# Performance work log

Measured on AMD Instinct MI355X. Metric: run time of the kernel, lower is better.

Reference implementation:

```python
import jax, jax.numpy as jnp
import numpy as np

N, E, B, EP = 100000, 1600000, 512, 200000
NIN, NEMB, HID, NL = 64, 64, 72, 3
EPS = 1e-5


def setup_inputs() -> dict:
    key = jax.random.key(0)
    ks = jax.random.split(key, 20)
    inp = {
        'x': jax.random.normal(ks[0], (N, NIN), jnp.float32),
        'emb': jax.random.normal(ks[1], (N, NEMB), jnp.float32),
        'assign': jax.random.uniform(ks[2], (N, B), jnp.float32),
        'edge_index': jax.random.randint(ks[3], (2, E), 0, N, jnp.int64),
        'pedge_index': jax.random.randint(ks[4], (2, EP), 0, B, jnp.int64),
        # params (xavier-ish scale)
        'node_w': jax.random.normal(ks[5], (NIN, HID), jnp.float32) / np.sqrt(NIN),
        'node_b': jnp.zeros((HID,), jnp.float32),
        'emb_w': jax.random.normal(ks[6], (NEMB, HID), jnp.float32) / np.sqrt(NEMB),
        'emb_b': jnp.zeros((HID,), jnp.float32),
        'conv_winit': jax.random.normal(ks[7], (NL, HID, HID), jnp.float32) / np.sqrt(HID),
        'conv_wroot': jax.random.normal(ks[8], (NL, HID, HID), jnp.float32) / np.sqrt(HID),
        'conv_bias': jnp.zeros((NL, HID), jnp.float32),
        'bn_gamma': jnp.ones((NL, HID), jnp.float32),
        'bn_beta': jnp.zeros((NL, HID), jnp.float32),
        'mlp_w1': jax.random.normal(ks[9], (12 * HID, HID), jnp.float32) / np.sqrt(12 * HID),
        'mlp_b1': jnp.zeros((HID,), jnp.float32),
        'mlp_w2': jax.random.normal(ks[10], (HID, 1), jnp.float32) / np.sqrt(HID),
        'mlp_b2': jnp.zeros((1,), jnp.float32),
    }
    return inp


def _forward(x, emb, assign, node_w, node_b, emb_w, emb_b, conv_winit,
             conv_wroot, conv_bias, bn_gamma, bn_beta, mlp_w1, mlp_b1,
             mlp_w2, mlp_b2, edge_index, pedge_index):
    n = x.shape[0]
    nb = assign.shape[1]
    row, col = edge_index[0], edge_index[1]
    # gcn_norm without self-loops (ARMAConv): D^{-1/2} A D^{-1/2}
    deg = jax.ops.segment_sum(jnp.ones((row.shape[0],), x.dtype), col, num_segments=n)
    dis = jnp.where(deg > 0, jax.lax.rsqrt(jnp.maximum(deg, 1.0)) * jnp.where(deg > 0, 1.0, 0.0), 0.0)
    dis = jnp.where(deg > 0, deg ** -0.5, 0.0)
    norm = dis[row] * dis[col]

    h = jax.nn.relu(x @ node_w + node_b)  # [N, HID]
    for l in range(NL):
        # ARMAConv K=1, T=1: relu(A_hat (h Wi) + h Wr + b)
        m = norm[:, None] * (h @ conv_winit[l])[row]        # [E, HID]
        agg = jax.ops.segment_sum(m, col, num_segments=n)   # [N, HID]
        h = jax.nn.relu(agg + h @ conv_wroot[l] + conv_bias[l])
        # F.relu applied again in forward (idempotent), then BatchNorm (training stats)
        mu = h.mean(0)
        var = ((h - mu) ** 2).mean(0)
        h = (h - mu) * jax.lax.rsqrt(var + EPS) * bn_gamma[l] + bn_beta[l]

    e = jax.nn.relu(emb @ emb_w + emb_b)
    z = jnp.concatenate([h, e], axis=-1)  # [N, 2*HID]

    batch = jnp.argmax(assign, axis=-1)
    cnt = jax.ops.segment_sum(jnp.ones((n,), z.dtype), batch, num_segments=nb)
    p1 = jax.ops.segment_sum(z, batch, num_segments=nb)
    p2 = jax.ops.segment_max(z, batch, num_segments=nb)
    p3 = p1 / jnp.maximum(cnt, 1.0)[:, None]
    xp = jnp.concatenate([p1, p2, p3], axis=-1)  # [B, 6*HID]

    pair = jnp.concatenate([xp[pedge_index[0]], xp[pedge_index[1]]], axis=1)  # [EP, 12*HID]
    out = jnp.tanh(pair @ mlp_w1 + mlp_b1) @ mlp_w2 + mlp_b2
    return out


def reference(x, emb, assign, edge_index, pedge_index, node_w, node_b, emb_w,
              emb_b, conv_winit, conv_wroot, conv_bias, bn_gamma, bn_beta,
              mlp_w1, mlp_b1, mlp_w2, mlp_b2):
    return _forward(x, emb, assign, node_w, node_b, emb_w, emb_b, conv_winit,
                    conv_wroot, conv_bias, bn_gamma, bn_beta, mlp_w1, mlp_b1,
                    mlp_w2, mlp_b2, edge_index, pedge_index)
```

## Files before the change

kernel.cpp:

```cpp
#include <hip/hip_runtime.h>
#include <hip/hip_bf16.h>

#define HID 72
#define EPSV 1e-5f
#define CAP 64

__device__ __forceinline__ float tanh_fast(float x) {
    float cx = fminf(fmaxf(x, -15.f), 15.f);
    float e = __expf(2.f * cx);
    return __fdividef(e - 1.f, e + 1.f);
}
__device__ __forceinline__ void fma4(float4& a, float w, const float4 v) {
    a.x += w * v.x; a.y += w * v.y; a.z += w * v.z; a.w += w * v.w;
}

__global__ void k_init(int* deg, float* stats, int* bcnt, int N, int statlen, int B) {
    int i = blockIdx.x * blockDim.x + threadIdx.x;
    if (i < N) deg[i] = 0;
    if (i < statlen) stats[i] = 0.f;
    if (i < B) bcnt[i] = 0;
}

__global__ __launch_bounds__(256) void k_fillcap(const int* __restrict__ row, const int* __restrict__ col,
                                                 int* __restrict__ deg, int* __restrict__ csr_r, int E) {
    int e = blockIdx.x * blockDim.x + threadIdx.x;
    if (e < E) {
        int c = col[e];
        int pos = atomicAdd(&deg[c], 1);
        if (pos < CAP) csr_r[(size_t)c * CAP + pos] = row[e];
    }
}

__global__ void k_dis(const int* __restrict__ deg, float* __restrict__ dis, int N) {
    int i = blockIdx.x * blockDim.x + threadIdx.x;
    if (i < N) {
        int d = deg[i];
        dis[i] = (d > 0) ? rsqrtf((float)d) : 0.f;
    }
}

#define DP 76
template <int K>
__global__ __launch_bounds__(256) void k_dense_t(const float* __restrict__ xin, const float* __restrict__ W,
                                                 const float* __restrict__ bias, float* __restrict__ out, int N) {
    __shared__ float hs[128][DP];
    __shared__ float ws[HID][DP];
    int tid = threadIdx.x;
    int n0 = blockIdx.x * 128;
    for (int i = tid; i < K * HID; i += 256) {
        int k = i / HID, f = i % HID;
        ws[f][k] = W[i];
    }
    for (int i = tid; i < 128 * K; i += 256) {
        int n = i / K, f = i % K;
        int gn = n0 + n;
        hs[n][f] = (gn < N) ? xin[(size_t)gn * K + f] : 0.f;
    }
    __syncthreads();
    int tn = tid & 31;
    int tf = (tid >> 5) * 9;
    float acc[4][9];
    #pragma unroll
    for (int j = 0; j < 9; j++) {
        float b = bias[tf + j];
        acc[0][j] = b; acc[1][j] = b; acc[2][j] = b; acc[3][j] = b;
    }
    #pragma unroll 2
    for (int k4 = 0; k4 < K / 4; k4++) {
        int k = k4 * 4;
        float4 h0 = *(const float4*)&hs[tn][k];
        float4 h1 = *(const float4*)&hs[tn + 32][k];
        float4 h2 = *(const float4*)&hs[tn + 64][k];
        float4 h3 = *(const float4*)&hs[tn + 96][k];
        #pragma unroll
        for (int j = 0; j < 9; j++) {
            float4 w = *(const float4*)&ws[tf + j][k];
            acc[0][j] += h0.x * w.x + h0.y * w.y + h0.z * w.z + h0.w * w.w;
            acc[1][j] += h1.x * w.x + h1.y * w.y + h1.z * w.z + h1.w * w.w;
            acc[2][j] += h2.x * w.x + h2.y * w.y + h2.z * w.z + h2.w * w.w;
            acc[3][j] += h3.x * w.x + h3.y * w.y + h3.z * w.z + h3.w * w.w;
        }
    }
    #pragma unroll
    for (int i = 0; i < 4; i++) {
        int gn = n0 + tn + 32 * i;
        if (gn >= N) continue;
        float* dst = out + (size_t)gn * HID + tf;
        #pragma unroll
        for (int j = 0; j < 9; j++) dst[j] = fmaxf(acc[i][j], 0.f);
    }
}

#define CP 76
template <bool BN>
__global__ __launch_bounds__(256) void k_conv_t(const float* t, const float* __restrict__ stats,
                                                const float* __restrict__ gamma, const float* __restrict__ beta,
                                                const float* __restrict__ wi, const float* __restrict__ wr,
                                                const float* __restrict__ cb, float* __restrict__ hw,
                                                float* agg, int N, float invN) {
    __shared__ float hs[64][CP];
    __shared__ float ws[2 * HID][CP];
    int tid = threadIdx.x;
    int n0 = blockIdx.x * 64;
    for (int i = tid; i < HID * 2 * HID; i += 256) {
        int k = i / (2 * HID), f = i % (2 * HID);
        ws[f][k] = (f < HID) ? wi[k * HID + f] : wr[k * HID + (f - HID)];
    }
    for (int i = tid; i < 64 * HID; i += 256) {
        int n = i / HID, f = i % HID;
        int gn = n0 + n;
        float v = (gn < N) ? t[(size_t)gn * HID + f] : 0.f;
        if constexpr (BN) {
            float mu = stats[f] * invN;
            float var = stats[HID + f] * invN - mu * mu;
            v = (v - mu) * rsqrtf(var + EPSV) * gamma[f] + beta[f];
        }
        hs[n][f] = v;
    }
    __syncthreads();
    int tn = tid & 15;
    int tf = (tid >> 4) * 9;
    float acc[4][9];
    #pragma unroll
    for (int j = 0; j < 9; j++) {
        float b = (tf >= HID) ? cb[tf - HID + j] : 0.f;
        acc[0][j] = b; acc[1][j] = b; acc[2][j] = b; acc[3][j] = b;
    }
    #pragma unroll 2
    for (int k4 = 0; k4 < HID / 4; k4++) {
        int k = k4 * 4;
        float4 h0 = *(const float4*)&hs[tn][k];
        float4 h1 = *(const float4*)&hs[tn + 16][k];
        float4 h2 = *(const float4*)&hs[tn + 32][k];
        float4 h3 = *(const float4*)&hs[tn + 48][k];
        #pragma unroll
        for (int j = 0; j < 9; j++) {
            float4 w = *(const float4*)&ws[tf + j][k];
            acc[0][j] += h0.x * w.x + h0.y * w.y + h0.z * w.z + h0.w * w.w;
            acc[1][j] += h1.x * w.x + h1.y * w.y + h1.z * w.z + h1.w * w.w;
            acc[2][j] += h2.x * w.x + h2.y * w.y + h2.z * w.z + h2.w * w.w;
            acc[3][j] += h3.x * w.x + h3.y * w.y + h3.z * w.z + h3.w * w.w;
        }
    }
    #pragma unroll
    for (int i = 0; i < 4; i++) {
        int gn = n0 + tn + 16 * i;
        if (gn >= N) continue;
        float* dst = (tf < HID) ? (hw + (size_t)gn * HID + tf) : (agg + (size_t)gn * HID + (tf - HID));
        #pragma unroll
        for (int j = 0; j < 9; j++) dst[j] = acc[i][j];
    }
}

__global__ __launch_bounds__(256) void k_gather9(const float* __restrict__ hw, const int* __restrict__ deg,
                                                 const int* __restrict__ csr_r, const float* __restrict__ dis,
                                                 float* t, int N) {
    int tid = blockIdx.x * blockDim.x + threadIdx.x;
    int n = tid / 9;
    int s = tid - n * 9;
    if (n >= N) return;
    float4* trow = (float4*)(t + (size_t)n * HID) + s * 2;
    float4 a0 = trow[0], a1 = trow[1];
    int d = deg[n];
    d = (d > CAP) ? CAP : d;
    float disc = dis[n];
    const int* crow = csr_r + (size_t)n * CAP;
    const float4* hb = (const float4*)hw + s * 2;
    for (int j0 = 0; j0 < d; j0 += 4) {
        int4 rr = *(const int4*)(crow + j0);
        int rem = d - j0;
        {
            float w = disc * dis[rr.x];
            const float4* hp = hb + (size_t)rr.x * 18;
            fma4(a0, w, hp[0]); fma4(a1, w, hp[1]);
        }
        if (rem > 1) {
            float w = disc * dis[rr.y];
            const float4* hp = hb + (size_t)rr.y * 18;
            fma4(a0, w, hp[0]); fma4(a1, w, hp[1]);
        }
        if (rem > 2) {
            float w = disc * dis[rr.z];
            const float4* hp = hb + (size_t)rr.z * 18;
            fma4(a0, w, hp[0]); fma4(a1, w, hp[1]);
        }
        if (rem > 3) {
            float w = disc * dis[rr.w];
            const float4* hp = hb + (size_t)rr.w * 18;
            fma4(a0, w, hp[0]); fma4(a1, w, hp[1]);
        }
    }
    trow[0] = make_float4(fmaxf(a0.x, 0.f), fmaxf(a0.y, 0.f), fmaxf(a0.z, 0.f), fmaxf(a0.w, 0.f));
    trow[1] = make_float4(fmaxf(a1.x, 0.f), fmaxf(a1.y, 0.f), fmaxf(a1.z, 0.f), fmaxf(a1.w, 0.f));
}

__global__ __launch_bounds__(256) void k_stats(const float* __restrict__ t, float* __restrict__ st, int total4) {
    __shared__ float s1[HID], s2[HID];
    int tx = threadIdx.x;
    if (tx < HID) s1[tx] = 0.f;
    else if (tx < 2 * HID) s2[tx - HID] = 0.f;
    __syncthreads();
    int stride = gridDim.x * blockDim.x;
    int i0 = blockIdx.x * blockDim.x + tx;
    int f0 = (i0 * 4) % HID;
    float a0 = 0, a1 = 0, a2 = 0, a3 = 0, q0 = 0, q1 = 0, q2 = 0, q3 = 0;
    const float4* tp = (const float4*)t;
    for (int i = i0; i < total4; i += stride) {
        float4 v = tp[i];
        a0 += v.x; q0 += v.x * v.x;
        a1 += v.y; q1 += v.y * v.y;
        a2 += v.z; q2 += v.z * v.z;
        a3 += v.w; q3 += v.w * v.w;
    }
    atomicAdd(&s1[f0 + 0], a0); atomicAdd(&s2[f0 + 0], q0);
    atomicAdd(&s1[f0 + 1], a1); atomicAdd(&s2[f0 + 1], q1);
    atomicAdd(&s1[f0 + 2], a2); atomicAdd(&s2[f0 + 2], q2);
    atomicAdd(&s1[f0 + 3], a3); atomicAdd(&s2[f0 + 3], q3);
    __syncthreads();
    if (tx < HID) {
        atomicAdd(&st[tx], s1[tx]);
        atomicAdd(&st[HID + tx], s2[tx]);
    }
}

__global__ __launch_bounds__(256) void k_argmax(const float* __restrict__ assign, int* __restrict__ batchv,
                                                int* __restrict__ bcnt, int N, int B) {
    int wib = threadIdx.x >> 6;
    int lane = threadIdx.x & 63;
    int n = blockIdx.x * (blockDim.x >> 6) + wib;
    if (n >= N) return;
    const float4* rp4 = (const float4*)(assign + (size_t)n * B);
    float best = -INFINITY;
    int bidx = 0x7fffffff;
    int nq = B / 4;
    for (int q = lane; q < nq; q += 64) {
        float4 v = rp4[q];
        int j = q * 4;
        if (v.x > best) { best = v.x; bidx = j; }
        if (v.y > best) { best = v.y; bidx = j + 1; }
        if (v.z > best) { best = v.z; bidx = j + 2; }
        if (v.w > best) { best = v.w; bidx = j + 3; }
    }
    #pragma unroll
    for (int off = 32; off > 0; off >>= 1) {
        float ov = __shfl_down(best, off);
        int oi = __shfl_down(bidx, off);
        if (ov > best || (ov == best && oi < bidx)) { best = ov; bidx = oi; }
    }
    if (lane == 0) {
        batchv[n] = bidx;
        atomicAdd(&bcnt[bidx], 1);
    }
}

__global__ __launch_bounds__(1024) void k_bscan(const int* __restrict__ bcnt, int* __restrict__ boffs,
                                                int* __restrict__ bcur, int B) {
    __shared__ int lds[1024];
    int t = threadIdx.x;
    int v = (t < B) ? bcnt[t] : 0;
    lds[t] = v;
    __syncthreads();
    for (int off = 1; off < 1024; off <<= 1) {
        int x = (t >= off) ? lds[t - off] : 0;
        __syncthreads();
        lds[t] += x;
        __syncthreads();
    }
    if (t < B) {
        int excl = lds[t] - v;
        boffs[t] = excl;
        bcur[t] = excl;
    }
}

__global__ void k_bfill(const int* __restrict__ batchv, int* __restrict__ bcur, int* __restrict__ nlist, int N) {
    int n = blockIdx.x * blockDim.x + threadIdx.x;
    if (n < N) {
        int b = batchv[n];
        int pos = atomicAdd(&bcur[b], 1);
        nlist[pos] = n;
    }
}

__global__ __launch_bounds__(576) void k_poolB(const float* __restrict__ t2, const float* __restrict__ ebuf,
                                               const float* __restrict__ stats2, const float* __restrict__ g2,
                                               const float* __restrict__ bt2, const int* __restrict__ boffs,
                                               const int* __restrict__ bcnt, const int* __restrict__ nlist,
                                               float* __restrict__ xp, float invN) {
    __shared__ float ls[4][2 * HID], lm[4][2 * HID];
    int b = blockIdx.x;
    int tid = threadIdx.x;
    int f = tid % (2 * HID);
    int ch = tid / (2 * HID);
    bool isH = f < HID;
    float a = 1.f, sh = 0.f;
    const float* src;
    if (isH) {
        float s1v = stats2[f], s2v = stats2[HID + f];
        float mu = s1v * invN;
        float var = s2v * invN - mu * mu;
        float inv = rsqrtf(var + EPSV);
        a = inv * g2[f];
        sh = bt2[f] - mu * a;
        src = t2 + f;
    } else {
        src = ebuf + (f - HID);
    }
    int s = boffs[b];
    int c = bcnt[b];
    int e = s + c;
    float sum = 0.f, mx = -INFINITY;
    for (int i = s + ch; i < e; i += 4) {
        float v = src[(size_t)nlist[i] * HID] * a + sh;
        sum += v;
        mx = fmaxf(mx, v);
    }
    ls[ch][f] = sum;
    lm[ch][f] = mx;
    __syncthreads();
    if (ch == 0) {
        float stot = ls[0][f] + ls[1][f] + ls[2][f] + ls[3][f];
        float mtot = fmaxf(fmaxf(lm[0][f], lm[1][f]), fmaxf(lm[2][f], lm[3][f]));
        float* xr = xp + (size_t)b * (6 * HID);
        xr[f] = stot;
        xr[2 * HID + f] = mtot;
        xr[4 * HID + f] = stot / fmaxf((float)c, 1.f);
    }
}

__global__ __launch_bounds__(192) void k_uv(const float* __restrict__ xp, const float* __restrict__ w1,
                                            const float* __restrict__ b1, float* __restrict__ U,
                                            float* __restrict__ V) {
    int b = blockIdx.x;
    int t = threadIdx.x;
    if (t >= 2 * HID) return;
    int half = t / HID;
    int f = t % HID;
    const float* xr = xp + (size_t)b * (6 * HID);
    const float* wb = w1 + (size_t)half * (6 * HID) * HID + f;
    float acc = (half == 0) ? b1[f] : 0.f;
    #pragma unroll 4
    for (int k = 0; k < 6 * HID; k++) acc += xr[k] * wb[(size_t)k * HID];
    if (half == 0) U[(size_t)b * HID + f] = acc;
    else           V[(size_t)b * HID + f] = acc;
}

__global__ __launch_bounds__(256) void k_edge(const int* __restrict__ pe, const float* __restrict__ U,
                                              const float* __restrict__ V, const float* __restrict__ w2,
                                              const float* __restrict__ b2, float* __restrict__ out, int EP) {
    int ep = blockIdx.x * blockDim.x + threadIdx.x;
    if (ep >= EP) return;
    int a = pe[ep];
    int b = pe[EP + ep];
    const float4* up = (const float4*)(U + (size_t)a * HID);
    const float4* vp = (const float4*)(V + (size_t)b * HID);
    float s = 0.f;
    #pragma unroll
    for (int q = 0; q < HID / 4; q++) {
        float4 u = up[q];
        float4 v = vp[q];
        s += tanh_fast(u.x + v.x) * w2[q * 4 + 0];
        s += tanh_fast(u.y + v.y) * w2[q * 4 + 1];
        s += tanh_fast(u.z + v.z) * w2[q * 4 + 2];
        s += tanh_fast(u.w + v.w) * w2[q * 4 + 3];
    }
    out[ep] = s + b2[0];
}

extern "C" void kernel_launch(void* const* d_in, const int* in_sizes, int n_in,
                              void* d_out, int out_size, void* d_ws, size_t ws_size,
                              hipStream_t stream) {
    const float* x       = (const float*)d_in[0];
    const float* emb     = (const float*)d_in[1];
    const float* assign  = (const float*)d_in[2];
    const int*   ei      = (const int*)d_in[3];
    const int*   pe      = (const int*)d_in[4];
    const float* node_w  = (const float*)d_in[5];
    const float* node_b  = (const float*)d_in[6];
    const float* emb_w   = (const float*)d_in[7];
    const float* emb_b   = (const float*)d_in[8];
    const float* conv_wi = (const float*)d_in[9];
    const float* conv_wr = (const float*)d_in[10];
    const float* conv_b  = (const float*)d_in[11];
    const float* bn_g    = (const float*)d_in[12];
    const float* bn_b    = (const float*)d_in[13];
    const float* w1      = (const float*)d_in[14];
    const float* b1      = (const float*)d_in[15];
    const float* w2      = (const float*)d_in[16];
    const float* b2      = (const float*)d_in[17];

    int N = in_sizes[0] / 64;
    int B = in_sizes[2] / N;
    int E = in_sizes[3] / 2;
    int EP = in_sizes[4] / 2;
    float invN = 1.0f / (float)N;

    char* wp = (char*)d_ws;
    auto alloc = [&](size_t nbytes) -> void* {
        void* p = (void*)wp;
        wp += (nbytes + 255) & ~(size_t)255;
        return p;
    };
    float* t_buf  = (float*)alloc((size_t)N * HID * 4);
    float* hw     = (float*)alloc((size_t)N * HID * 4);
    float* e_buf  = (float*)alloc((size_t)N * HID * 4);
    int*   csr_r  = (int*)alloc((size_t)N * CAP * 4);
    int*   deg    = (int*)alloc((size_t)N * 4);
    float* dis    = (float*)alloc((size_t)N * 4);
    int*   batchv = (int*)alloc((size_t)N * 4);
    int*   nlist  = (int*)alloc((size_t)N * 4);
    float* stats  = (float*)alloc((size_t)3 * 2 * HID * 4);
    int*   bcnt   = (int*)alloc((size_t)B * 4);
    int*   boffs  = (int*)alloc((size_t)B * 4);
    int*   bcur   = (int*)alloc((size_t)B * 4);
    float* xp     = (float*)alloc((size_t)B * 6 * HID * 4);
    float* Ub     = (float*)alloc((size_t)B * HID * 4);
    float* Vb     = (float*)alloc((size_t)B * HID * 4);

    const int* row = ei;
    const int* col = ei + E;

    int nb256_N = (N + 255) / 256;
    int nb256_E = (E + 255) / 256;

    k_init<<<nb256_N, 256, 0, stream>>>(deg, stats, bcnt, N, 3 * 2 * HID, B);
    k_fillcap<<<nb256_E, 256, 0, stream>>>(row, col, deg, csr_r, E);
    k_dis<<<nb256_N, 256, 0, stream>>>(deg, dis, N);

    k_dense_t<64><<<(N + 127) / 128, 256, 0, stream>>>(x, node_w, node_b, t_buf, N);
    k_dense_t<64><<<(N + 127) / 128, 256, 0, stream>>>(emb, emb_w, emb_b, e_buf, N);

    for (int l = 0; l < 3; l++) {
        const float* wi = conv_wi + (size_t)l * HID * HID;
        const float* wr = conv_wr + (size_t)l * HID * HID;
        const float* cb = conv_b + (size_t)l * HID;
        if (l == 0)
            k_conv_t<false><<<(N + 63) / 64, 256, 0, stream>>>(t_buf, nullptr, nullptr, nullptr,
                                                               wi, wr, cb, hw, t_buf, N, invN);
        else
            k_conv_t<true><<<(N + 63) / 64, 256, 0, stream>>>(t_buf, stats + (size_t)(l - 1) * 2 * HID,
                                                              bn_g + (size_t)(l - 1) * HID,
                                                              bn_b + (size_t)(l - 1) * HID,
                                                              wi, wr, cb, hw, t_buf, N, invN);
        k_gather9<<<(9 * N + 255) / 256, 256, 0, stream>>>(hw, deg, csr_r, dis, t_buf, N);
        k_stats<<<288, 256, 0, stream>>>(t_buf, stats + (size_t)l * 2 * HID, N * HID / 4);
    }

    k_argmax<<<(N + 3) / 4, 256, 0, stream>>>(assign, batchv, bcnt, N, B);
    k_bscan<<<1, 1024, 0, stream>>>(bcnt, boffs, bcur, B);
    k_bfill<<<nb256_N, 256, 0, stream>>>(batchv, bcur, nlist, N);
    k_poolB<<<B, 576, 0, stream>>>(t_buf, e_buf, stats + (size_t)2 * 2 * HID,
                                   bn_g + (size_t)2 * HID, bn_b + (size_t)2 * HID,
                                   boffs, bcnt, nlist, xp, invN);
    k_uv<<<B, 192, 0, stream>>>(xp, w1, b1, Ub, Vb);
    k_edge<<<(EP + 255) / 256, 256, 0, stream>>>(pe, Ub, Vb, w2, b2, (float*)d_out, EP);
}
```

Measured before the change: 1.325 ms.

## Merge CSR fill, input projections and argmax into one front kernel

Four independent front-end kernels (CSR fill with degree atomics, two dense input projections, argmax over the assignment matrix) are combined into one launch, with the block range deciding each block's role, so the independent work can overlap on the device. The CSR fill now handles eight edges per thread using int4 loads. The dense part reads inputs straight from global memory instead of staging them in LDS. The dis computation moves into the first conv kernel. This cuts launch gaps and lets the memory-bound argmax overlap the atomic-heavy fill, though mixed block roles can give uneven scheduling.

Result: faster. 1.287 ms (-2.8%).

```diff
diff --git a/kernel.cpp b/kernel.cpp
--- a/kernel.cpp
+++ b/kernel.cpp
@@ -4,6 +4,8 @@
 #define HID 72
 #define EPSV 1e-5f
 #define CAP 64
+#define DP 76
+#define GF 1024
 
 __device__ __forceinline__ float tanh_fast(float x) {
     float cx = fminf(fmaxf(x, -15.f), 15.f);
@@ -21,87 +23,148 @@
     if (i < B) bcnt[i] = 0;
 }
 
-__global__ __launch_bounds__(256) void k_fillcap(const int* __restrict__ row, const int* __restrict__ col,
-                                                 int* __restrict__ deg, int* __restrict__ csr_r, int E) {
-    int e = blockIdx.x * blockDim.x + threadIdx.x;
-    if (e < E) {
-        int c = col[e];
-        int pos = atomicAdd(&deg[c], 1);
-        if (pos < CAP) csr_r[(size_t)c * CAP + pos] = row[e];
-    }
-}
-
-__global__ void k_dis(const int* __restrict__ deg, float* __restrict__ dis, int N) {
-    int i = blockIdx.x * blockDim.x + threadIdx.x;
-    if (i < N) {
-        int d = deg[i];
-        dis[i] = (d > 0) ? rsqrtf((float)d) : 0.f;
-    }
-}
-
-#define DP 76
-template <int K>
-__global__ __launch_bounds__(256) void k_dense_t(const float* __restrict__ xin, const float* __restrict__ W,
-                                                 const float* __restrict__ bias, float* __restrict__ out, int N) {
-    __shared__ float hs[128][DP];
+__global__ __launch_bounds__(256) void k_front(const int* __restrict__ row, const int* __restrict__ col,
+                                               int* __restrict__ deg, int* __restrict__ csr_r, int E,
+                                               const float* __restrict__ x, const float* __restrict__ node_w,
+                                               const float* __restrict__ node_b, float* __restrict__ t_buf,
+                                               const float* __restrict__ emb, const float* __restrict__ emb_w,
+                                               const float* __restrict__ emb_b, float* __restrict__ e_buf,
+                                               const float* __restrict__ assign, int* __restrict__ batchv,
+                                               int* __restrict__ bcnt, int N, int B, int GD) {
     __shared__ float ws[HID][DP];
     int tid = threadIdx.x;
-    int n0 = blockIdx.x * 128;
-    for (int i = tid; i < K * HID; i += 256) {
-        int k = i / HID, f = i % HID;
-        ws[f][k] = W[i];
-    }
-    for (int i = tid; i < 128 * K; i += 256) {
-        int n = i / K, f = i % K;
-        int gn = n0 + n;
-        hs[n][f] = (gn < N) ? xin[(size_t)gn * K + f] : 0.f;
-    }
-    __syncthreads();
-    int tn = tid & 31;
-    int tf = (tid >> 5) * 9;
-    float acc[4][9];
-    #pragma unroll
-    for (int j = 0; j < 9; j++) {
-        float b = bias[tf + j];
-        acc[0][j] = b; acc[1][j] = b; acc[2][j] = b; acc[3][j] = b;
-    }
-    #pragma unroll 2
-    for (int k4 = 0; k4 < K / 4; k4++) {
-        int k = k4 * 4;
-        float4 h0 = *(const float4*)&hs[tn][k];
-        float4 h1 = *(const float4*)&hs[tn + 32][k];
-        float4 h2 = *(const float4*)&hs[tn + 64][k];
-        float4 h3 = *(const float4*)&hs[tn + 96][k];
+    int bid = blockIdx.x;
+
+    if (bid < GF) {
+        int stride = GF * 256 * 8;
+        for (int base = (bid * 256 + tid) * 8; base < E; base += stride) {
+            #pragma unroll
+            for (int h = 0; h < 2; h++) {
+                int eb = base + h * 4;
+                if (eb + 3 < E) {
+                    int4 cc = *(const int4*)(col + eb);
+                    int4 rr = *(const int4*)(row + eb);
+                    int p0 = atomicAdd(&deg[cc.x], 1);
+                    int p1 = atomicAdd(&deg[cc.y], 1);
+                    int p2 = atomicAdd(&deg[cc.z], 1);
+                    int p3 = atomicAdd(&deg[cc.w], 1);
+                    if (p0 < CAP) csr_r[(size_t)cc.x * CAP + p0] = rr.x;
+                    if (p1 < CAP) csr_r[(size_t)cc.y * CAP + p1] = rr.y;
+                    if (p2 < CAP) csr_r[(size_t)cc.z * CAP + p2] = rr.z;
+                    if (p3 < CAP) csr_r[(size_t)cc.w * CAP + p3] = rr.w;
+                } else if (eb < E) {
+                    int lim = (eb + 4 < E) ? eb + 4 : E;
+                    for (int e = eb; e < lim; e++) {
+                        int c = col[e];
+                        int pos = atomicAdd(&deg[c], 1);
+                        if (pos < CAP) csr_r[(size_t)c * CAP + pos] = row[e];
+                    }
+                }
+            }
+        }
+        return;
+    }
+    bid -= GF;
+    if (bid < 2 * GD) {
+        const float* xin; const float* W; const float* bias; float* out;
+        int tb = bid;
+        if (tb < GD) { xin = x;   W = node_w; bias = node_b; out = t_buf; }
+        else         { xin = emb; W = emb_w;  bias = emb_b;  out = e_buf; tb -= GD; }
+        int n0 = tb * 128;
+        for (int i = tid; i < 64 * HID; i += 256) {
+            int k = i / HID, f = i % HID;
+            ws[f][k] = W[i];
+        }
+        __syncthreads();
+        int tn = tid & 31;
+        int tf = (tid >> 5) * 9;
+        float acc[4][9];
         #pragma unroll
         for (int j = 0; j < 9; j++) {
-            float4 w = *(const float4*)&ws[tf + j][k];
-            acc[0][j] += h0.x * w.x + h0.y * w.y + h0.z * w.z + h0.w * w.w;
-            acc[1][j] += h1.x * w.x + h1.y * w.y + h1.z * w.z + h1.w * w.w;
-            acc[2][j] += h2.x * w.x + h2.y * w.y + h2.z * w.z + h2.w * w.w;
-            acc[3][j] += h3.x * w.x + h3.y * w.y + h3.z * w.z + h3.w * w.w;
-        }
+            float b = bias[tf + j];
+            acc[0][j] = b; acc[1][j] = b; acc[2][j] = b; acc[3][j] = b;
+        }
+        int g0 = n0 + tn;
+        const float4* xp0 = (const float4*)(xin + (size_t)(g0      < N ? g0      : N - 1) * 64);
+        const float4* xp1 = (const float4*)(xin + (size_t)(g0 + 32 < N ? g0 + 32 : N - 1) * 64);
+        const float4* xp2 = (const float4*)(xin + (size_t)(g0 + 64 < N ? g0 + 64 : N - 1) * 64);
+        const float4* xp3 = (const float4*)(xin + (size_t)(g0 + 96 < N ? g0 + 96 : N - 1) * 64);
+        #pragma unroll 2
+        for (int k4 = 0; k4 < 16; k4++) {
+            float4 h0 = xp0[k4];
+            float4 h1 = xp1[k4];
+            float4 h2 = xp2[k4];
+            float4 h3 = xp3[k4];
+            int k = k4 * 4;
+            #pragma unroll
+            for (int j = 0; j < 9; j++) {
+                float4 w = *(const float4*)&ws[tf + j][k];
+                acc[0][j] += h0.x * w.x + h0.y * w.y + h0.z * w.z + h0.w * w.w;
+                acc[1][j] += h1.x * w.x + h1.y * w.y + h1.z * w.z + h1.w * w.w;
+                acc[2][j] += h2.x * w.x + h2.y * w.y + h2.z * w.z + h2.w * w.w;
+                acc[3][j] += h3.x * w.x + h3.y * w.y + h3.z * w.z + h3.w * w.w;
+            }
+        }
+        #pragma unroll
+        for (int i = 0; i < 4; i++) {
+            int gn = n0 + tn + 32 * i;
+            if (gn >= N) continue;
+            float* dst = out + (size_t)gn * HID + tf;
+            #pragma unroll
+            for (int j = 0; j < 9; j++) dst[j] = fmaxf(acc[i][j], 0.f);
+        }
+        return;
+    }
+    bid -= 2 * GD;
+    int wib = tid >> 6;
+    int lane = tid & 63;
+    int n = bid * 4 + wib;
+    if (n >= N) return;
+    const float4* rp4 = (const float4*)(assign + (size_t)n * B);
+    float best = -INFINITY;
+    int bidx = 0x7fffffff;
+    int nq = B / 4;
+    for (int q = lane; q < nq; q += 64) {
+        float4 v = rp4[q];
+        int j = q * 4;
+        if (v.x > best) { best = v.x; bidx = j; }
+        if (v.y > best) { best = v.y; bidx = j + 1; }
+        if (v.z > best) { best = v.z; bidx = j + 2; }
+        if (v.w > best) { best = v.w; bidx = j + 3; }
     }
     #pragma unroll
-    for (int i = 0; i < 4; i++) {
-        int gn = n0 + tn + 32 * i;
-        if (gn >= N) continue;
-        float* dst = out + (size_t)gn * HID + tf;
-        #pragma unroll
-        for (int j = 0; j < 9; j++) dst[j] = fmaxf(acc[i][j], 0.f);
+    for (int off = 32; off > 0; off >>= 1) {
+        float ov = __shfl_down(best, off);
+        int oi = __shfl_down(bidx, off);
+        if (ov > best || (ov == best && oi < bidx)) { best = ov; bidx = oi; }
+    }
+    if (lane == 0) {
+        batchv[n] = bidx;
+        atomicAdd(&bcnt[bidx], 1);
     }
 }
 
 #define CP 76
-template <bool BN>
+template <bool BN, bool DIS>
 __global__ __launch_bounds__(256) void k_conv_t(const float* t, const float* __restrict__ stats,
                                                 const float* __restrict__ gamma, const float* __restrict__ beta,
                                                 const float* __restrict__ wi, const float* __restrict__ wr,
                                                 const float* __restrict__ cb, float* __restrict__ hw,
-                                                float* agg, int N, float invN) {
+                                                float* agg, int N, float invN,
+                                                const int* __restrict__ deg, float* __restrict__ dis) {
     __shared__ float hs[64][CP];
     __shared__ float ws[2 * HID][CP];
     int tid = threadIdx.x;
     int n0 = blockIdx.x * 64;
+    if constexpr (DIS) {
+        if (tid < 64) {
+            int gn = n0 + tid;
+            if (gn < N) {
+                int d = deg[gn];
+                dis[gn] = (d > 0) ? rsqrtf((float)d) : 0.f;
+            }
+        }
+    }
     for (int i = tid; i < HID * 2 * HID; i += 256) {
         int k = i / (2 * HID), f = i % (2 * HID);
         ws[f][k] = (f < HID) ? wi[k * HID + f] : wr[k * HID + (f - HID)];
@@ -220,36 +283,6 @@
     if (tx < HID) {
         atomicAdd(&st[tx], s1[tx]);
         atomicAdd(&st[HID + tx], s2[tx]);
-    }
-}
-
-__global__ __launch_bounds__(256) void k_argmax(const float* __restrict__ assign, int* __restrict__ batchv,
-                                                int* __restrict__ bcnt, int N, int B) {
-    int wib = threadIdx.x >> 6;
-    int lane = threadIdx.x & 63;
-    int n = blockIdx.x * (blockDim.x >> 6) + wib;
-    if (n >= N) return;
-    const float4* rp4 = (const float4*)(assign + (size_t)n * B);
-    float best = -INFINITY;
-    int bidx = 0x7fffffff;
-    int nq = B / 4;
-    for (int q = lane; q < nq; q += 64) {
-        float4 v = rp4[q];
-        int j = q * 4;
-        if (v.x > best) { best = v.x; bidx = j; }
-        if (v.y > best) { best = v.y; bidx = j + 1; }
-        if (v.z > best) { best = v.z; bidx = j + 2; }
-        if (v.w > best) { best = v.w; bidx = j + 3; }
-    }
-    #pragma unroll
-    for (int off = 32; off > 0; off >>= 1) {
-        float ov = __shfl_down(best, off);
-        int oi = __shfl_down(bidx, off);
-        if (ov > best || (ov == best && oi < bidx)) { best = ov; bidx = oi; }
-    }
-    if (lane == 0) {
-        batchv[n] = bidx;
-        atomicAdd(&bcnt[bidx], 1);
     }
 }
 
@@ -421,32 +454,34 @@
     const int* col = ei + E;
 
     int nb256_N = (N + 255) / 256;
-    int nb256_E = (E + 255) / 256;
+    int GD = (N + 127) / 128;
+    int GA = (N + 3) / 4;
 
     k_init<<<nb256_N, 256, 0, stream>>>(deg, stats, bcnt, N, 3 * 2 * HID, B);
-    k_fillcap<<<nb256_E, 256, 0, stream>>>(row, col, deg, csr_r, E);
-    k_dis<<<nb256_N, 256, 0, stream>>>(deg, dis, N);
-
-    k_dense_t<64><<<(N + 127) / 128, 256, 0, stream>>>(x, node_w, node_b, t_buf, N);
-    k_dense_t<64><<<(N + 127) / 128, 256, 0, stream>>>(emb, emb_w, emb_b, e_buf, N);
+
+    k_front<<<GF + 2 * GD + GA, 256, 0, stream>>>(row, col, deg, csr_r, E,
+                                                  x, node_w, node_b, t_buf,
+                                                  emb, emb_w, emb_b, e_buf,
+                                                  assign, batchv, bcnt, N, B, GD);
 
     for (int l = 0; l < 3; l++) {
         const float* wi = conv_wi + (size_t)l * HID * HID;
         const float* wr = conv_wr + (size_t)l * HID * HID;
         const float* cb = conv_b + (size_t)l * HID;
         if (l == 0)
-            k_conv_t<false><<<(N + 63) / 64, 256, 0, stream>>>(t_buf, nullptr, nullptr, nullptr,
-                                                               wi, wr, cb, hw, t_buf, N, invN);
+            k_conv_t<false, true><<<(N + 63) / 64, 256, 0, stream>>>(t_buf, nullptr, nullptr, nullptr,
+                                                                     wi, wr, cb, hw, t_buf, N, invN,
+                                                                     deg, dis);
         else
-            k_conv_t<true><<<(N + 63) / 64, 256, 0, stream>>>(t_buf, stats + (size_t)(l - 1) * 2 * HID,
-                                                              bn_g + (size_t)(l - 1) * HID,
-                                                              bn_b + (size_t)(l - 1) * HID,
-                                                              wi, wr, cb, hw, t_buf, N, invN);
+            k_conv_t<true, false><<<(N + 63) / 64, 256, 0, stream>>>(t_buf, stats + (size_t)(l - 1) * 2 * HID,
+                                                                     bn_g + (size_t)(l - 1) * HID,
+                                                                     bn_b + (size_t)(l - 1) * HID,
+                                                                     wi, wr, cb, hw, t_buf, N, invN,
+                                                                     nullptr, nullptr);
         k_gather9<<<(9 * N + 255) / 256, 256, 0, stream>>>(hw, deg, csr_r, dis, t_buf, N);
         k_stats<<<288, 256, 0, stream>>>(t_buf, stats + (size_t)l * 2 * HID, N * HID / 4);
     }
 
-    k_argmax<<<(N + 3) / 4, 256, 0, stream>>>(assign, batchv, bcnt, N, B);
     k_bscan<<<1, 1024, 0, stream>>>(bcnt, boffs, bcur, B);
     k_bfill<<<nb256_N, 256, 0, stream>>>(batchv, bcur, nlist, N);
     k_poolB<<<B, 576, 0, stream>>>(t_buf, e_buf, stats + (size_t)2 * 2 * HID,
```
